# Kernel tuning notes

Hardware: AMD Instinct MI355X
Metric: run time of the kernel (lower is better)

## Reference

```python
import jax, jax.numpy as jnp
import numpy as np


def setup_inputs() -> dict:
    key = jax.random.key(0)
    ks = jax.random.split(key, 7)
    B, EN, DE, E, U, T = 8, 512, 64, 512, 512, 100  # batch, max_words, max_label, emb, units, topics
    return {
        "en_seq": jax.random.normal(ks[0], (B, EN, E), dtype=jnp.float32),
        "de_seq": jax.random.normal(ks[1], (B, DE, E), dtype=jnp.float32),
        "topics": jax.random.uniform(ks[2], (B, T), dtype=jnp.float32),
        "w_en": jax.random.normal(ks[3], (E, U), dtype=jnp.float32) * 0.05,
        "w_de": jax.random.normal(ks[4], (E, U), dtype=jnp.float32) * 0.05,
        "nu": jax.random.normal(ks[5], (U,), dtype=jnp.float32) * 0.05,
        "wt": jax.random.normal(ks[6], (E, T), dtype=jnp.float32) * 0.05,
    }


def reference(en_seq, de_seq, topics, w_en, w_de, nu, wt):
    # Additive (Bahdanau-style) attention with a per-batch topic bias.
    att_en = jnp.einsum("bie,eu->biu", en_seq, w_en)        # [B, EN, U]
    att_de = jnp.einsum("bje,eu->bju", de_seq, w_de)        # [B, DE, U]
    topics_w = jnp.einsum("bt,ut->bu", topics, wt)          # [B, U] (wt is [E,U-dim? no: E==U])
    # co_m[b, j, i, u] = att_en[b,i,u] + att_de[b,j,u] + topics_w[b,u]
    co_m = jnp.tanh(att_en[:, None, :, :] + att_de[:, :, None, :]
                    + topics_w[:, None, None, :])           # [B, DE, EN, U]
    mu = jnp.einsum("bjiu,u->bji", co_m, nu)                # [B, DE, EN]
    alphas = jax.nn.softmax(mu, axis=-1)                    # softmax over encoder positions
    p_gen = jax.nn.sigmoid(mu)
    sum_en = jnp.einsum("bji,bie->bje", alphas, en_seq)     # attention-weighted encoder sum
    output = de_seq + sum_en
    return (output, alphas, p_gen)
```

## Files before the change

kernel.cpp:

```cpp
#include <hip/hip_runtime.h>
#include <hip/hip_bf16.h>

#define NB  8
#define ENW 512
#define DEW 64
#define EMB 512
#define UN  512
#define NT  100

#define KSCALE 2.8853900817779268f
#define L2E    1.4426950408889634f

typedef short bf16x8 __attribute__((ext_vector_type(8)));
typedef unsigned short u16x8 __attribute__((ext_vector_type(8)));
typedef float f32x4  __attribute__((ext_vector_type(4)));

__device__ __forceinline__ unsigned short f2bf(float f) {
    union { float f; unsigned int u; } v; v.f = f;
    unsigned int r = v.u + 0x7FFFu + ((v.u >> 16) & 1u);
    return (unsigned short)(r >> 16);
}

__global__ __launch_bounds__(256) void prep_kernel(const float* __restrict__ w_en,
                                                   const float* __restrict__ w_de,
                                                   const float* __restrict__ en,
                                                   const float* __restrict__ de,
                                                   const float* __restrict__ topics,
                                                   const float* __restrict__ wt_mat,
                                                   const float* __restrict__ nu,
                                                   unsigned short* __restrict__ wen_t,
                                                   unsigned short* __restrict__ wde_t,
                                                   unsigned short* __restrict__ en_bf,
                                                   unsigned short* __restrict__ de_bf,
                                                   float* __restrict__ tw2,
                                                   float* __restrict__ snu,
                                                   float* __restrict__ nu2) {
    const int bx = blockIdx.x, t = threadIdx.x;
    if (bx < 128) {
        __shared__ float tile[64][65];
        const float* w = (bx < 64) ? w_en : w_de;
        unsigned short* o = (bx < 64) ? wen_t : wde_t;
        const int tb = bx & 63;
        const int r0 = (tb >> 3) * 64;
        const int c0 = (tb & 7) * 64;
        const int rr = t >> 4, cc = (t & 15) * 4;
#pragma unroll
        for (int q = 0; q < 4; ++q) {
            float4 v = *(const float4*)(w + (size_t)(r0 + rr + 16 * q) * 512 + c0 + cc);
            *(float4*)&tile[rr + 16 * q][cc] = v;
        }
        __syncthreads();
#pragma unroll
        for (int q = 0; q < 4; ++q) {
            int ul = rr + 16 * q;
            int el = cc;
            ushort4 v;
            v.x = f2bf(KSCALE * tile[el][ul]);
            v.y = f2bf(KSCALE * tile[el + 1][ul]);
            v.z = f2bf(KSCALE * tile[el + 2][ul]);
            v.w = f2bf(KSCALE * tile[el + 3][ul]);
            *(ushort4*)(o + (size_t)(c0 + ul) * 512 + r0 + el) = v;
        }
    } else if (bx < 1280) {
        const bool is_en = (bx < 1152);
        const float* src = is_en ? en : de;
        unsigned short* dst = is_en ? en_bf : de_bf;
        const int idx = ((is_en ? (bx - 128) : (bx - 1152)) * 256 + t) * 8;
        float4 a0 = *(const float4*)(src + idx);
        float4 a1 = *(const float4*)(src + idx + 4);
        u16x8 o;
        o[0] = f2bf(a0.x); o[1] = f2bf(a0.y); o[2] = f2bf(a0.z); o[3] = f2bf(a0.w);
        o[4] = f2bf(a1.x); o[5] = f2bf(a1.y); o[6] = f2bf(a1.z); o[7] = f2bf(a1.w);
        *(u16x8*)(dst + idx) = o;
    } else if (bx < 1296) {
        int idx = (bx - 1280) * 256 + t;
        int b = idx >> 9, u = idx & 511;
        const float* tp = topics + b * NT;
        const float* wp = wt_mat + u * NT;
        float s = 0.f;
        for (int tt = 0; tt < NT; ++tt) s += tp[tt] * wp[tt];
        tw2[idx] = KSCALE * s;
    } else {
        __shared__ float red[256];
        float n0 = nu[t], n1 = nu[t + 256];
        nu2[t] = -2.f * n0;
        nu2[t + 256] = -2.f * n1;
        red[t] = n0 + n1;
        __syncthreads();
        for (int off = 128; off > 0; off >>= 1) {
            if (t < off) red[t] += red[t + off];
            __syncthreads();
        }
        if (t == 0) snu[0] = red[0];
    }
}

__global__ __launch_bounds__(256) void gemm_fused(const unsigned short* __restrict__ en_bf,
                                                  const unsigned short* __restrict__ de_bf,
                                                  const unsigned short* __restrict__ wen_t,
                                                  const unsigned short* __restrict__ wde_t,
                                                  const float* __restrict__ tw2,
                                                  float* __restrict__ Ea,
                                                  float* __restrict__ Eb) {
    const int K = 512, N = 512;
    const int bx = blockIdx.x;
    const bool is_de = (bx >= 64);
    const unsigned short* A = is_de ? de_bf : en_bf;
    const unsigned short* Bt = is_de ? wde_t : wen_t;
    float* C = is_de ? Eb : Ea;
    const int mb = is_de ? (bx - 64) : bx;

    const int lane = threadIdx.x & 63;
    const int wave = threadIdx.x >> 6;
    const int m0 = mb * 64 + wave * 16;
    const int n0 = blockIdx.y * 64;
    const int row = m0 + (lane & 15);
    const int kq  = (lane >> 4) * 8;

    f32x4 acc[4];
#pragma unroll
    for (int nn = 0; nn < 4; ++nn) acc[nn] = 0.f;

    const unsigned short* ap = A + (size_t)row * K + kq;
    const unsigned short* bp = Bt + (size_t)(n0 + (lane & 15)) * K + kq;
#pragma unroll 4
    for (int kc = 0; kc < K; kc += 32) {
        bf16x8 a = *(const bf16x8*)(ap + kc);
#pragma unroll
        for (int nn = 0; nn < 4; ++nn) {
            bf16x8 b = *(const bf16x8*)(bp + (size_t)nn * 16 * K + kc);
            acc[nn] = __builtin_amdgcn_mfma_f32_16x16x32_bf16(a, b, acc[nn], 0, 0, 0);
        }
    }
    const int crow = m0 + (lane >> 4) * 4;
    const int ccol = lane & 15;
#pragma unroll
    for (int nn = 0; nn < 4; ++nn)
#pragma unroll
        for (int r = 0; r < 4; ++r) {
            int rw = crow + r, cl = n0 + nn * 16 + ccol;
            float v = acc[nn][r];
            if (is_de) v += tw2[(rw >> 6) * 512 + cl];
            C[(size_t)rw * N + cl] = __builtin_amdgcn_exp2f(v);
        }
}

__global__ __launch_bounds__(256) void mu4_kernel(const float* __restrict__ Ea,
                                                  const float* __restrict__ Eb,
                                                  const float* __restrict__ nu2,
                                                  const float* __restrict__ snu,
                                                  float* __restrict__ mu) {
    __shared__ float As[16][132];
    __shared__ float Bs[16][132];
    __shared__ float Ns[512];
    const int t = threadIdx.x;
    const int bx = blockIdx.x;
    const int jg = bx & 3;
    const int isplit = (bx >> 2) & 31;
    const int b = bx >> 7;
    const int i0 = isplit * 16, j0 = jg * 16;
    const int il = t & 15, jr = t >> 4;

    Ns[t] = nu2[t];
    Ns[t + 256] = nu2[t + 256];

    const float* aeb = Ea + (size_t)(b * ENW + i0) * UN;
    const float* bib = Eb + (size_t)(b * DEW + j0) * UN;

    float s0 = 0.f, s1 = 0.f;
    for (int uc = 0; uc < 512; uc += 128) {
#pragma unroll
        for (int q = 0; q < 2; ++q) {
            int idx = q * 256 + t;
            int row = idx >> 5, c4 = idx & 31;
            float4 va = *(const float4*)(aeb + (size_t)row * UN + uc + c4 * 4);
            *(float4*)&As[row][c4 * 4] = va;
            float4 vb = *(const float4*)(bib + (size_t)row * UN + uc + c4 * 4);
            *(float4*)&Bs[row][c4 * 4] = vb;
        }
        __syncthreads();
#pragma unroll 8
        for (int c = 0; c < 32; ++c) {
            float4 a  = *(const float4*)&As[il][c * 4];
            float4 bb = *(const float4*)&Bs[jr][c * 4];
            float4 nv = *(const float4*)&Ns[uc + c * 4];
            float e0 = fmaf(a.x, bb.x, 1.f);
            float e1 = fmaf(a.y, bb.y, 1.f);
            float e2 = fmaf(a.z, bb.z, 1.f);
            float e3 = fmaf(a.w, bb.w, 1.f);
            s0 = fmaf(nv.x, __builtin_amdgcn_rcpf(e0), s0);
            s1 = fmaf(nv.y, __builtin_amdgcn_rcpf(e1), s1);
            s0 = fmaf(nv.z, __builtin_amdgcn_rcpf(e2), s0);
            s1 = fmaf(nv.w, __builtin_amdgcn_rcpf(e3), s1);
        }
        __syncthreads();
    }
    mu[(size_t)(b * DEW + j0 + jr) * ENW + i0 + il] = snu[0] + s0 + s1;
}

__global__ __launch_bounds__(256) void softfin_kernel(const float* __restrict__ mu,
                                                      const float* __restrict__ en,
                                                      const float* __restrict__ de,
                                                      float* __restrict__ out,
                                                      float* __restrict__ alphas,
                                                      float* __restrict__ p_gen) {
    __shared__ float Al[4][512];
    __shared__ float Ps[4][4][256];
    const int bx = blockIdx.x;
    const int eh = bx & 1;
    const int jq = (bx >> 1) & 15;
    const int b  = bx >> 5;
    const int t = threadIdx.x;
    const int wave = t >> 6, lane = t & 63;
    const int j0 = jq * 4;

    {
        const int bj = b * DEW + j0 + wave;
        const float* mup = mu + (size_t)bj * ENW;
        float v[8], a[8];
#pragma unroll
        for (int c = 0; c < 8; ++c) v[c] = mup[c * 64 + lane];
        float mx = v[0];
#pragma unroll
        for (int c = 1; c < 8; ++c) mx = fmaxf(mx, v[c]);
#pragma unroll
        for (int off = 32; off > 0; off >>= 1) mx = fmaxf(mx, __shfl_xor(mx, off));
        float s = 0.f;
#pragma unroll
        for (int c = 0; c < 8; ++c) { a[c] = __builtin_amdgcn_exp2f((v[c] - mx) * L2E); s += a[c]; }
#pragma unroll
        for (int off = 32; off > 0; off >>= 1) s += __shfl_xor(s, off);
        float inv = __builtin_amdgcn_rcpf(s);
#pragma unroll
        for (int c = 0; c < 8; ++c) {
            a[c] *= inv;
            Al[wave][c * 64 + lane] = a[c];
        }
        if (eh == 0) {
            float* alp = alphas + (size_t)bj * ENW;
            float* pgp = p_gen + (size_t)bj * ENW;
#pragma unroll
            for (int c = 0; c < 8; ++c) {
                alp[c * 64 + lane] = a[c];
                pgp[c * 64 + lane] = __builtin_amdgcn_rcpf(1.f + __builtin_amdgcn_exp2f(-v[c] * L2E));
            }
        }
    }
    __syncthreads();

    const int i0 = wave * 128;
    const float* enb = en + (size_t)b * ENW * EMB + eh * 256 + lane * 4;
    f32x4 acc[4];
#pragma unroll
    for (int jj = 0; jj < 4; ++jj) acc[jj] = 0.f;
    for (int ig = 0; ig < 128; ig += 4) {
        const int ib = i0 + ig;
        float4 al0 = *(const float4*)&Al[0][ib];
        float4 al1 = *(const float4*)&Al[1][ib];
        float4 al2 = *(const float4*)&Al[2][ib];
        float4 al3 = *(const float4*)&Al[3][ib];
#pragma unroll
        for (int r = 0; r < 4; ++r) {
            float4 x = *(const float4*)(enb + (size_t)(ib + r) * EMB);
            float w0 = (r == 0) ? al0.x : (r == 1) ? al0.y : (r == 2) ? al0.z : al0.w;
            float w1 = (r == 0) ? al1.x : (r == 1) ? al1.y : (r == 2) ? al1.z : al1.w;
            float w2 = (r == 0) ? al2.x : (r == 1) ? al2.y : (r == 2) ? al2.z : al2.w;
            float w3 = (r == 0) ? al3.x : (r == 1) ? al3.y : (r == 2) ? al3.z : al3.w;
            acc[0][0] = fmaf(w0, x.x, acc[0][0]); acc[0][1] = fmaf(w0, x.y, acc[0][1]);
            acc[0][2] = fmaf(w0, x.z, acc[0][2]); acc[0][3] = fmaf(w0, x.w, acc[0][3]);
            acc[1][0] = fmaf(w1, x.x, acc[1][0]); acc[1][1] = fmaf(w1, x.y, acc[1][1]);
            acc[1][2] = fmaf(w1, x.z, acc[1][2]); acc[1][3] = fmaf(w1, x.w, acc[1][3]);
            acc[2][0] = fmaf(w2, x.x, acc[2][0]); acc[2][1] = fmaf(w2, x.y, acc[2][1]);
            acc[2][2] = fmaf(w2, x.z, acc[2][2]); acc[2][3] = fmaf(w2, x.w, acc[2][3]);
            acc[3][0] = fmaf(w3, x.x, acc[3][0]); acc[3][1] = fmaf(w3, x.y, acc[3][1]);
            acc[3][2] = fmaf(w3, x.z, acc[3][2]); acc[3][3] = fmaf(w3, x.w, acc[3][3]);
        }
    }
#pragma unroll
    for (int jj = 0; jj < 4; ++jj)
        *(f32x4*)&Ps[wave][jj][lane * 4] = acc[jj];
    __syncthreads();

    {
        const int bj = b * DEW + j0 + wave;
        const int e = eh * 256 + lane * 4;
        float4 p0 = *(const float4*)&Ps[0][wave][lane * 4];
        float4 p1 = *(const float4*)&Ps[1][wave][lane * 4];
        float4 p2 = *(const float4*)&Ps[2][wave][lane * 4];
        float4 p3 = *(const float4*)&Ps[3][wave][lane * 4];
        float4 d = *(const float4*)(de + (size_t)bj * EMB + e);
        float4 o;
        o.x = d.x + (p0.x + p1.x) + (p2.x + p3.x);
        o.y = d.y + (p0.y + p1.y) + (p2.y + p3.y);
        o.z = d.z + (p0.z + p1.z) + (p2.z + p3.z);
        o.w = d.w + (p0.w + p1.w) + (p2.w + p3.w);
        *(float4*)(out + (size_t)bj * EMB + e) = o;
    }
}

extern "C" void kernel_launch(void* const* d_in, const int* in_sizes, int n_in,
                              void* d_out, int out_size, void* d_ws, size_t ws_size,
                              hipStream_t stream) {
    const float* en     = (const float*)d_in[0];
    const float* de     = (const float*)d_in[1];
    const float* topics = (const float*)d_in[2];
    const float* w_en   = (const float*)d_in[3];
    const float* w_de   = (const float*)d_in[4];
    const float* nu     = (const float*)d_in[5];
    const float* wt     = (const float*)d_in[6];

    float* out    = (float*)d_out;
    float* alphas = out + 262144;
    float* p_gen  = out + 524288;

    char* ws = (char*)d_ws;
    float* Ea             = (float*)(ws);
    float* Eb             = (float*)(ws + 8388608);
    float* tw2            = (float*)(ws + 9437184);
    float* mu             = (float*)(ws + 9453568);
    unsigned short* en_bf = (unsigned short*)(ws + 10502144);
    unsigned short* de_bf = (unsigned short*)(ws + 14696448);
    unsigned short* wen_t = (unsigned short*)(ws + 15220736);
    unsigned short* wde_t = (unsigned short*)(ws + 15745024);
    float* snu            = (float*)(ws + 16269312);
    float* nu2            = (float*)(ws + 16269328);

    prep_kernel<<<1297, 256, 0, stream>>>(w_en, w_de, en, de, topics, wt, nu,
                                          wen_t, wde_t, en_bf, de_bf, tw2, snu, nu2);
    gemm_fused<<<dim3(72, 8), 256, 0, stream>>>(en_bf, de_bf, wen_t, wde_t, tw2, Ea, Eb);
    mu4_kernel<<<1024, 256, 0, stream>>>(Ea, Eb, nu2, snu, mu);
    softfin_kernel<<<256, 256, 0, stream>>>(mu, en, de, out, alphas, p_gen);
}
```

Before: 142.3 us.

## Stage GEMM weights in swizzled LDS and retile mu kernel with U-split partials

The GEMM now loads each block's 64x512 bf16 weight tile into LDS with direct global-to-LDS loads and an XOR swizzle, instead of every wave re-reading it from global memory. The mu kernel is retiled so each thread computes four encoder positions, reusing the decoder row from LDS across them. The unit dimension is split in two, and the softmax kernel sums the two partial mu buffers and adds the constant. The workspace is reshuffled so the mu buffers alias en_bf, which is dead by then. This adds 64KB of LDS to the GEMM, which may limit occupancy, and an extra partial-buffer read in softmax.

```diff
diff --git a/kernel.cpp b/kernel.cpp
--- a/kernel.cpp
+++ b/kernel.cpp
@@ -14,6 +14,10 @@
 typedef short bf16x8 __attribute__((ext_vector_type(8)));
 typedef unsigned short u16x8 __attribute__((ext_vector_type(8)));
 typedef float f32x4  __attribute__((ext_vector_type(4)));
+
+#define GLOAD_LDS16(src, dst) __builtin_amdgcn_global_load_lds( \
+    (const __attribute__((address_space(1))) void*)(src),       \
+    (__attribute__((address_space(3))) void*)(dst), 16, 0, 0)
 
 __device__ __forceinline__ unsigned short f2bf(float f) {
     union { float f; unsigned int u; } v; v.f = f;
@@ -102,6 +106,7 @@
                                                   const float* __restrict__ tw2,
                                                   float* __restrict__ Ea,
                                                   float* __restrict__ Eb) {
+    __shared__ unsigned short Blds[64 * 512];
     const int K = 512, N = 512;
     const int bx = blockIdx.x;
     const bool is_de = (bx >= 64);
@@ -112,23 +117,34 @@
 
     const int lane = threadIdx.x & 63;
     const int wave = threadIdx.x >> 6;
+    const int n0 = blockIdx.y * 64;
+
+#pragma unroll
+    for (int q = 0; q < 16; ++q) {
+        const int R = wave * 16 + q;
+        const unsigned short* src = Bt + (size_t)(n0 + R) * K + ((lane * 8) ^ ((R & 7) << 3));
+        GLOAD_LDS16(src, &Blds[R * 512]);
+    }
+
     const int m0 = mb * 64 + wave * 16;
-    const int n0 = blockIdx.y * 64;
     const int row = m0 + (lane & 15);
     const int kq  = (lane >> 4) * 8;
+    const int nrow = lane & 15;
+    const int swz = (nrow & 7) << 3;
 
     f32x4 acc[4];
 #pragma unroll
     for (int nn = 0; nn < 4; ++nn) acc[nn] = 0.f;
 
     const unsigned short* ap = A + (size_t)row * K + kq;
-    const unsigned short* bp = Bt + (size_t)(n0 + (lane & 15)) * K + kq;
+    __syncthreads();
 #pragma unroll 4
     for (int kc = 0; kc < K; kc += 32) {
         bf16x8 a = *(const bf16x8*)(ap + kc);
+        const int col = (kq + kc) ^ swz;
 #pragma unroll
         for (int nn = 0; nn < 4; ++nn) {
-            bf16x8 b = *(const bf16x8*)(bp + (size_t)nn * 16 * K + kc);
+            bf16x8 b = *(const bf16x8*)&Blds[(nrow + nn * 16) * 512 + col];
             acc[nn] = __builtin_amdgcn_mfma_f32_16x16x32_bf16(a, b, acc[nn], 0, 0, 0);
         }
     }
@@ -145,60 +161,80 @@
         }
 }
 
-__global__ __launch_bounds__(256) void mu4_kernel(const float* __restrict__ Ea,
+__global__ __launch_bounds__(256) void mu5_kernel(const float* __restrict__ Ea,
                                                   const float* __restrict__ Eb,
                                                   const float* __restrict__ nu2,
-                                                  const float* __restrict__ snu,
-                                                  float* __restrict__ mu) {
-    __shared__ float As[16][132];
+                                                  float* __restrict__ mu0,
+                                                  float* __restrict__ mu1) {
+    __shared__ float As[64][132];
     __shared__ float Bs[16][132];
-    __shared__ float Ns[512];
     const int t = threadIdx.x;
     const int bx = blockIdx.x;
-    const int jg = bx & 3;
-    const int isplit = (bx >> 2) & 31;
-    const int b = bx >> 7;
-    const int i0 = isplit * 16, j0 = jg * 16;
+    const int us = bx & 1;
+    const int it = (bx >> 1) & 7;
+    const int jt = (bx >> 4) & 3;
+    const int b  = bx >> 6;
+    const int i0 = it * 64, j0 = jt * 16, u0 = us * 256;
     const int il = t & 15, jr = t >> 4;
 
-    Ns[t] = nu2[t];
-    Ns[t + 256] = nu2[t + 256];
-
     const float* aeb = Ea + (size_t)(b * ENW + i0) * UN;
-    const float* bib = Eb + (size_t)(b * DEW + j0) * UN;
-
-    float s0 = 0.f, s1 = 0.f;
-    for (int uc = 0; uc < 512; uc += 128) {
+    const float* beb = Eb + (size_t)(b * DEW + j0) * UN;
+
+    float s0 = 0.f, s1 = 0.f, s2 = 0.f, s3 = 0.f;
+#pragma unroll
+    for (int half = 0; half < 2; ++half) {
+        const int uc = u0 + half * 128;
+#pragma unroll
+        for (int q = 0; q < 8; ++q) {
+            int idx = q * 256 + t;
+            int rowi = idx >> 5, c4 = idx & 31;
+            *(float4*)&As[rowi][c4 * 4] = *(const float4*)(aeb + (size_t)rowi * UN + uc + c4 * 4);
+        }
 #pragma unroll
         for (int q = 0; q < 2; ++q) {
             int idx = q * 256 + t;
-            int row = idx >> 5, c4 = idx & 31;
-            float4 va = *(const float4*)(aeb + (size_t)row * UN + uc + c4 * 4);
-            *(float4*)&As[row][c4 * 4] = va;
-            float4 vb = *(const float4*)(bib + (size_t)row * UN + uc + c4 * 4);
-            *(float4*)&Bs[row][c4 * 4] = vb;
+            int rowi = idx >> 5, c4 = idx & 31;
+            *(float4*)&Bs[rowi][c4 * 4] = *(const float4*)(beb + (size_t)rowi * UN + uc + c4 * 4);
         }
         __syncthreads();
 #pragma unroll 8
         for (int c = 0; c < 32; ++c) {
-            float4 a  = *(const float4*)&As[il][c * 4];
             float4 bb = *(const float4*)&Bs[jr][c * 4];
-            float4 nv = *(const float4*)&Ns[uc + c * 4];
-            float e0 = fmaf(a.x, bb.x, 1.f);
-            float e1 = fmaf(a.y, bb.y, 1.f);
-            float e2 = fmaf(a.z, bb.z, 1.f);
-            float e3 = fmaf(a.w, bb.w, 1.f);
-            s0 = fmaf(nv.x, __builtin_amdgcn_rcpf(e0), s0);
-            s1 = fmaf(nv.y, __builtin_amdgcn_rcpf(e1), s1);
-            s0 = fmaf(nv.z, __builtin_amdgcn_rcpf(e2), s0);
-            s1 = fmaf(nv.w, __builtin_amdgcn_rcpf(e3), s1);
+            float4 nv = *(const float4*)(nu2 + uc + c * 4);
+            float4 a0 = *(const float4*)&As[il][c * 4];
+            float4 a1 = *(const float4*)&As[il + 16][c * 4];
+            float4 a2 = *(const float4*)&As[il + 32][c * 4];
+            float4 a3 = *(const float4*)&As[il + 48][c * 4];
+            s0 = fmaf(nv.x, __builtin_amdgcn_rcpf(fmaf(a0.x, bb.x, 1.f)), s0);
+            s0 = fmaf(nv.y, __builtin_amdgcn_rcpf(fmaf(a0.y, bb.y, 1.f)), s0);
+            s0 = fmaf(nv.z, __builtin_amdgcn_rcpf(fmaf(a0.z, bb.z, 1.f)), s0);
+            s0 = fmaf(nv.w, __builtin_amdgcn_rcpf(fmaf(a0.w, bb.w, 1.f)), s0);
+            s1 = fmaf(nv.x, __builtin_amdgcn_rcpf(fmaf(a1.x, bb.x, 1.f)), s1);
+            s1 = fmaf(nv.y, __builtin_amdgcn_rcpf(fmaf(a1.y, bb.y, 1.f)), s1);
+            s1 = fmaf(nv.z, __builtin_amdgcn_rcpf(fmaf(a1.z, bb.z, 1.f)), s1);
+            s1 = fmaf(nv.w, __builtin_amdgcn_rcpf(fmaf(a1.w, bb.w, 1.f)), s1);
+            s2 = fmaf(nv.x, __builtin_amdgcn_rcpf(fmaf(a2.x, bb.x, 1.f)), s2);
+            s2 = fmaf(nv.y, __builtin_amdgcn_rcpf(fmaf(a2.y, bb.y, 1.f)), s2);
+            s2 = fmaf(nv.z, __builtin_amdgcn_rcpf(fmaf(a2.z, bb.z, 1.f)), s2);
+            s2 = fmaf(nv.w, __builtin_amdgcn_rcpf(fmaf(a2.w, bb.w, 1.f)), s2);
+            s3 = fmaf(nv.x, __builtin_amdgcn_rcpf(fmaf(a3.x, bb.x, 1.f)), s3);
+            s3 = fmaf(nv.y, __builtin_amdgcn_rcpf(fmaf(a3.y, bb.y, 1.f)), s3);
+            s3 = fmaf(nv.z, __builtin_amdgcn_rcpf(fmaf(a3.z, bb.z, 1.f)), s3);
+            s3 = fmaf(nv.w, __builtin_amdgcn_rcpf(fmaf(a3.w, bb.w, 1.f)), s3);
         }
         __syncthreads();
     }
-    mu[(size_t)(b * DEW + j0 + jr) * ENW + i0 + il] = snu[0] + s0 + s1;
-}
-
-__global__ __launch_bounds__(256) void softfin_kernel(const float* __restrict__ mu,
+    float* mo = us ? mu1 : mu0;
+    const size_t base = (size_t)(b * DEW + j0 + jr) * ENW + i0 + il;
+    mo[base]      = s0;
+    mo[base + 16] = s1;
+    mo[base + 32] = s2;
+    mo[base + 48] = s3;
+}
+
+__global__ __launch_bounds__(256) void softfin_kernel(const float* __restrict__ mu0,
+                                                      const float* __restrict__ mu1,
+                                                      const float* __restrict__ snu,
                                                       const float* __restrict__ en,
                                                       const float* __restrict__ de,
                                                       float* __restrict__ out,
@@ -213,13 +249,15 @@
     const int t = threadIdx.x;
     const int wave = t >> 6, lane = t & 63;
     const int j0 = jq * 4;
+    const float snu0 = snu[0];
 
     {
         const int bj = b * DEW + j0 + wave;
-        const float* mup = mu + (size_t)bj * ENW;
+        const float* mup0 = mu0 + (size_t)bj * ENW;
+        const float* mup1 = mu1 + (size_t)bj * ENW;
         float v[8], a[8];
 #pragma unroll
-        for (int c = 0; c < 8; ++c) v[c] = mup[c * 64 + lane];
+        for (int c = 0; c < 8; ++c) v[c] = mup0[c * 64 + lane] + mup1[c * 64 + lane] + snu0;
         float mx = v[0];
 #pragma unroll
         for (int c = 1; c < 8; ++c) mx = fmaxf(mx, v[c]);
@@ -253,6 +291,7 @@
     f32x4 acc[4];
 #pragma unroll
     for (int jj = 0; jj < 4; ++jj) acc[jj] = 0.f;
+#pragma unroll 2
     for (int ig = 0; ig < 128; ig += 4) {
         const int ib = i0 + ig;
         float4 al0 = *(const float4*)&Al[0][ib];
@@ -317,17 +356,18 @@
     float* Ea             = (float*)(ws);
     float* Eb             = (float*)(ws + 8388608);
     float* tw2            = (float*)(ws + 9437184);
-    float* mu             = (float*)(ws + 9453568);
-    unsigned short* en_bf = (unsigned short*)(ws + 10502144);
-    unsigned short* de_bf = (unsigned short*)(ws + 14696448);
-    unsigned short* wen_t = (unsigned short*)(ws + 15220736);
-    unsigned short* wde_t = (unsigned short*)(ws + 15745024);
-    float* snu            = (float*)(ws + 16269312);
-    float* nu2            = (float*)(ws + 16269328);
+    unsigned short* en_bf = (unsigned short*)(ws + 9453568);
+    float* mu0            = (float*)(ws + 9453568);
+    float* mu1            = (float*)(ws + 10502144);
+    unsigned short* de_bf = (unsigned short*)(ws + 13647872);
+    unsigned short* wen_t = (unsigned short*)(ws + 14172160);
+    unsigned short* wde_t = (unsigned short*)(ws + 14696448);
+    float* snu            = (float*)(ws + 15220736);
+    float* nu2            = (float*)(ws + 15220752);
 
     prep_kernel<<<1297, 256, 0, stream>>>(w_en, w_de, en, de, topics, wt, nu,
                                           wen_t, wde_t, en_bf, de_bf, tw2, snu, nu2);
     gemm_fused<<<dim3(72, 8), 256, 0, stream>>>(en_bf, de_bf, wen_t, wde_t, tw2, Ea, Eb);
-    mu4_kernel<<<1024, 256, 0, stream>>>(Ea, Eb, nu2, snu, mu);
-    softfin_kernel<<<256, 256, 0, stream>>>(mu, en, de, out, alphas, p_gen);
-}
+    mu5_kernel<<<512, 256, 0, stream>>>(Ea, Eb, nu2, mu0, mu1);
+    softfin_kernel<<<256, 256, 0, stream>>>(mu0, mu1, snu, en, de, out, alphas, p_gen);
+}
```

Measured after the change: 122.3 us. 14.0% less time.
